# Kernel optimization log

Measured on AMD Instinct MI355X. Metric: run time of the kernel, lower is better.

Reference implementation:

```python
import jax, jax.numpy as jnp
import numpy as np

# KWConv2d config: in=256, out=256, k=3, s=1, p=1, groups=1, bias=False
# warehouse: 32 spatial cells of shape [64, 64, 3, 3]; num_fourier_basis=0; temp_value=0
B, CIN, H, W_ = 32, 256, 56, 56
OUT = 256
NUM_CELLS, CO, CI, KH, KW = 32, 64, 64, 3, 3
HIDDEN = 16                 # max(int(256 * 0.0625), 16)
GO, GI, GS = OUT // CO, CIN // CI, 1
M = GO * GI * GS            # num_local_mixture = 16
P = NUM_CELLS + 1           # kw_planes_per_mixture = 33
KWP = P * M                 # kw_planes = 528


def setup_inputs() -> dict:
    key = jax.random.key(0)
    ks = jax.random.split(key, 4)
    s = 0.02
    return {
        "x": jax.random.normal(ks[0], (B, CIN, H, W_), jnp.float32),
        "cells": jax.random.normal(ks[1], (NUM_CELLS, CO, CI, KH, KW), jnp.float32) * s,
        "fc1_w": jax.random.normal(ks[2], (HIDDEN, CIN), jnp.float32) * s,
        "fc1_b": jnp.zeros((HIDDEN,), jnp.float32),
        "ln_g": jnp.ones((HIDDEN,), jnp.float32),
        "ln_b": jnp.zeros((HIDDEN,), jnp.float32),
        "sp_w": jax.random.normal(ks[3], (KWP, HIDDEN), jnp.float32) * s,
        "sp_b": jnp.zeros((KWP,), jnp.float32),
    }


def _attention(x, fc1_w, fc1_b, ln_g, ln_b, sp_w, sp_b):
    # AdaptiveAvgPool1d(1) over flattened spatial dims == global mean
    pooled = x.mean(axis=(2, 3))                      # [B, CIN]
    h = pooled @ fc1_w.T + fc1_b                      # [B, HIDDEN]
    mu = h.mean(-1, keepdims=True)
    var = ((h - mu) ** 2).mean(-1, keepdims=True)
    h = (h - mu) * jax.lax.rsqrt(var + 1e-5) * ln_g + ln_b
    h = jax.nn.relu(h)
    a = h @ sp_w.T + sp_b                             # spatial_head -> [B, KWP]
    a = a.reshape(-1, P)                              # [B*M, P]
    a = a / (jnp.abs(a).sum(axis=1, keepdims=True) + 0.001)  # L1 normalize per mixture
    # temp_value = 0 -> attention unchanged; drop last (zero) column
    return a[:, :-1]                                  # [B*M, NUM_CELLS]


def reference(x, cells, fc1_w, fc1_b, ln_g, ln_b, sp_w, sp_b):
    att = _attention(x, fc1_w, fc1_b, ln_g, ln_b, sp_w, sp_b)  # [B*M, NUM_CELLS]
    w = cells.reshape(NUM_CELLS, -1)                  # [NUM_CELLS, CO*CI*KH*KW]
    agg = att @ w                                     # [B*M, CO*CI*KH*KW]
    agg = agg.reshape(B, GS, GO, GI, CO, CI, KH, KW)
    agg = agg.transpose(0, 2, 4, 3, 5, 1, 6, 7)       # torch permute (0,2,4,3,5,1,6,7)
    agg = agg.reshape(B * OUT, CIN, KH, KW)           # per-sample kernels (groups=1)
    # grouped-conv trick: fold batch into channels, groups = B
    xr = x.reshape(1, B * CIN, H, W_)
    out = jax.lax.conv_general_dilated(
        xr, agg, window_strides=(1, 1), padding=((1, 1), (1, 1)),
        dimension_numbers=("NCHW", "OIHW", "NCHW"), feature_group_count=B)
    return out.reshape(B, OUT, H, W_)
```

## Files before the change

kernel.cpp:

```cpp
#include <hip/hip_runtime.h>
#include <stdint.h>

typedef unsigned short ush;
typedef __bf16   bf16x8 __attribute__((ext_vector_type(8)));
typedef float    f32x4  __attribute__((ext_vector_type(4)));
typedef uint32_t u32x4  __attribute__((ext_vector_type(4)));

union U16B { u32x4 u; bf16x8 b; };
union P8   { ush us[8]; u32x4 v; };

__device__ __forceinline__ ush f2bf(float f) {
    union { float f; uint32_t u; } v; v.f = f;
    uint32_t r = v.u + 0x7FFFu + ((v.u >> 16) & 1u);
    return (ush)(r >> 16);
}

__device__ __forceinline__ void gl_lds16(const ush* g, ush* l) {
    __builtin_amdgcn_global_load_lds(
        (const __attribute__((address_space(1))) uint32_t*)g,
        (__attribute__((address_space(3))) uint32_t*)l, 16, 0, 0);
}

#define HWPX  3136
#define POOL_OFF   58720256UL
#define ATT_OFF    58753024UL
#define WAGG_OFF   58818560UL

__global__ void k_halo(u32x4* __restrict__ xT16, u32x4* __restrict__ pooled16) {
    int i = blockIdx.x * 256 + threadIdx.x;
    int rl = i >> 3, s = i & 7;
    u32x4 z = (u32x4)(0u);
    size_t byte = (size_t)rl * 4096 + (s < 4 ? s * 16 : 3648 + (s - 4) * 16);
    xT16[byte >> 4] = z;
    if (blockIdx.x < 8) pooled16[blockIdx.x * 256 + threadIdx.x] = z;
}

__global__ void k_transpose(const float* __restrict__ x, ush* __restrict__ xT,
                            float* __restrict__ pooled) {
    __shared__ float tile[64][65];
    int blk = blockIdx.x;
    int b   = blk / 196;
    int rem = blk % 196;
    int icg = rem / 49;
    int pxg = rem % 49;
    int t = threadIdx.x;

    {
        int icl  = t >> 2, part = t & 3;
        const float* src = x + (size_t)(b * 256 + icg * 64 + icl) * HWPX + pxg * 64 + part * 16;
        #pragma unroll
        for (int k = 0; k < 4; ++k) {
            f32x4 v = *(const f32x4*)(src + k * 4);
            tile[icl][part * 16 + k * 4 + 0] = v[0];
            tile[icl][part * 16 + k * 4 + 1] = v[1];
            tile[icl][part * 16 + k * 4 + 2] = v[2];
            tile[icl][part * 16 + k * 4 + 3] = v[3];
        }
    }
    __syncthreads();

    if (t < 64) {
        float s = 0.f;
        #pragma unroll 8
        for (int p = 0; p < 64; ++p) s += tile[t][p];
        atomicAdd(pooled + b * 256 + icg * 64 + t, s);
    }

    {
        int pxl = t >> 2, icq = t & 3;
        int px  = pxg * 64 + pxl;
        int row = px / 56;
        int col = px - row * 56;
        int p   = col + 1;
        int xorp = (p >> 1) & 3;
        int icg32   = icg * 2 + (icq >> 1);
        int subbase = (icq & 1) * 2;
        P8 lo, hi;
        #pragma unroll
        for (int m = 0; m < 8; ++m) {
            lo.us[m] = f2bf(tile[icq * 16 + m][pxl]);
            hi.us[m] = f2bf(tile[icq * 16 + 8 + m][pxl]);
        }
        size_t base = (((size_t)(b * 8 + icg32) * 56 + row) * 64 + p) * 32;
        *(u32x4*)(xT + base + (size_t)((subbase ^ xorp) * 8))       = lo.v;
        *(u32x4*)(xT + base + (size_t)(((subbase + 1) ^ xorp) * 8)) = hi.v;
    }
}

__global__ void k_attn(const float* __restrict__ pooled,
                       const float* __restrict__ fc1_w, const float* __restrict__ fc1_b,
                       const float* __restrict__ ln_g,  const float* __restrict__ ln_b,
                       const float* __restrict__ sp_w,  const float* __restrict__ sp_b,
                       float* __restrict__ att) {
    __shared__ float hs[32][16];
    int t = threadIdx.x;
    {
        int b = t >> 4, j = t & 15;
        float acc = 0.f;
        for (int c = 0; c < 256; ++c) acc += pooled[b * 256 + c] * fc1_w[j * 256 + c];
        hs[b][j] = fc1_b[j] + acc * (1.0f / 3136.0f);
    }
    __syncthreads();
    if (t < 32) {
        float mu = 0.f;
        #pragma unroll
        for (int j = 0; j < 16; ++j) mu += hs[t][j];
        mu *= (1.0f / 16.0f);
        float var = 0.f;
        #pragma unroll
        for (int j = 0; j < 16; ++j) { float d = hs[t][j] - mu; var += d * d; }
        var *= (1.0f / 16.0f);
        float inv = rsqrtf(var + 1e-5f);
        #pragma unroll
        for (int j = 0; j < 16; ++j) {
            float v = (hs[t][j] - mu) * inv * ln_g[j] + ln_b[j];
            hs[t][j] = fmaxf(v, 0.f);
        }
    }
    __syncthreads();
    {
        int b = t >> 4, m = t & 15;
        float a[33];
        #pragma unroll 1
        for (int i = 0; i < 33; ++i) {
            int p = m * 33 + i;
            float acc = sp_b[p];
            #pragma unroll
            for (int j = 0; j < 16; ++j) acc += hs[b][j] * sp_w[p * 16 + j];
            a[i] = acc;
        }
        float s = 0.f;
        #pragma unroll
        for (int i = 0; i < 33; ++i) s += fabsf(a[i]);
        float inv = 1.0f / (s + 0.001f);
        #pragma unroll
        for (int c = 0; c < 32; ++c) att[(b * 16 + m) * 32 + c] = a[c] * inv;
    }
}

__global__ void k_agg(const float* __restrict__ cells, const float* __restrict__ att,
                      ush* __restrict__ wagg) {
    __shared__ float at[512];
    int blk = blockIdx.x;
    int b = blk >> 6, co = blk & 63;
    int t = threadIdx.x;
    for (int i = t; i < 512; i += 256) at[i] = att[b * 512 + i];
    __syncthreads();
    int ci = t & 63, gi = t >> 6;
    float acc[4][9];
    #pragma unroll
    for (int g = 0; g < 4; ++g)
        #pragma unroll
        for (int k = 0; k < 9; ++k) acc[g][k] = 0.f;
    for (int c = 0; c < 32; ++c) {
        float a0 = at[(0 + gi) * 32 + c];
        float a1 = at[(4 + gi) * 32 + c];
        float a2 = at[(8 + gi) * 32 + c];
        float a3 = at[(12 + gi) * 32 + c];
        const float* cp = cells + (size_t)c * 36864 + co * 576 + ci * 9;
        #pragma unroll
        for (int k = 0; k < 9; ++k) {
            float cv = cp[k];
            acc[0][k] += a0 * cv; acc[1][k] += a1 * cv;
            acc[2][k] += a2 * cv; acc[3][k] += a3 * cv;
        }
    }
    #pragma unroll
    for (int g = 0; g < 4; ++g)
        #pragma unroll
        for (int k = 0; k < 9; ++k)
            wagg[((size_t)(b * 9 + k) * 256 + g * 64 + co) * 256 + gi * 64 + ci] = f2bf(acc[g][k]);
}

__global__ __launch_bounds__(256, 2) void k_conv(const ush* __restrict__ xT,
                                                 const ush* __restrict__ wagg,
                                                 float* __restrict__ out) {
    __shared__ __align__(16) ush xs[20480];
    __shared__ __align__(16) ush wsh[18432];

    int tid = threadIdx.x;
    int wg  = blockIdx.x;
    int xcd = wg & 7;
    int kk  = wg >> 3;
    int gq  = kk / 7;
    int sp  = kk - gq * 7;
    int g   = gq * 8 + xcd;
    int b   = g >> 2, octile = g & 3;
    int row0 = sp * 8, oc0 = octile * 64;

    int lane = tid & 63, w = tid >> 6;
    int l15 = lane & 15, s4 = lane >> 4;

    {
        u32x4 z = (u32x4)(0u);
        #pragma unroll
        for (int i = 0; i < 10; ++i) ((u32x4*)xs)[tid + i * 256] = z;
    }

    int prow[7], pq[7];
    #pragma unroll
    for (int j = 0; j < 7; ++j) {
        int px = w * 112 + j * 16 + l15;
        prow[j] = px / 56;
        pq[j]   = px - prow[j] * 56;
    }

    unsigned vmask = 0;
    #pragma unroll
    for (int k = 0; k < 10; ++k) {
        int grow = row0 - 1 + k;
        if (grow >= 0 && grow < 56) vmask |= 1u << k;
    }

    const ush* wgl = wagg + (size_t)b * 9 * 65536 + (size_t)(oc0 + (tid >> 2)) * 256 + (tid & 3) * 8;
    ush* wdst = wsh + ((tid & 3) * 64 + (tid >> 2)) * 8;
    const ush* wrd = wsh + (s4 * 64 + l15) * 8;
    const ush* xb = xT + (size_t)b * 8 * 56 * 2048 + (size_t)tid * 8;

    f32x4 acc[4][7];
    #pragma unroll
    for (int mi = 0; mi < 4; ++mi)
        #pragma unroll
        for (int j = 0; j < 7; ++j) acc[mi][j] = (f32x4)(0.f);

    __syncthreads();

    if ((wg >> 8) & 1) __builtin_amdgcn_s_sleep(32);

    for (int cc = 0; cc < 8; ++cc) {
        U16B wst[9];
        const ush* wcg = wgl + (size_t)cc * 32;
        #pragma unroll
        for (int k = 0; k < 9; ++k) wst[k].u = *(const u32x4*)(wcg + (size_t)k * 65536);
        #pragma unroll
        for (int k = 0; k < 10; ++k)
            if (vmask & (1u << k))
                gl_lds16(xb + (size_t)(cc * 56 + row0 - 1 + k) * 2048, xs + k * 2048 + w * 512);
        #pragma unroll
        for (int k = 0; k < 9; ++k) *(u32x4*)(wdst + k * 2048) = wst[k].u;
        __syncthreads();

        #pragma unroll
        for (int tap = 0; tap < 9; ++tap) {
            const int dy = tap / 3, dx = tap % 3;
            U16B wf[4];
            #pragma unroll
            for (int mi = 0; mi < 4; ++mi)
                wf[mi].u = *(const u32x4*)(wrd + tap * 2048 + mi * 128);
            U16B bx[7];
            #pragma unroll
            for (int j = 0; j < 7; ++j) {
                int q    = pq[j] + dx;
                int slot = s4 ^ ((q >> 1) & 3);
                bx[j].u = *(const u32x4*)(xs + ((prow[j] + dy) * 64 + q) * 32 + slot * 8);
            }
            __builtin_amdgcn_s_setprio(1);
            #pragma unroll
            for (int j = 0; j < 7; ++j) {
                acc[0][j] = __builtin_amdgcn_mfma_f32_16x16x32_bf16(bx[j].b, wf[0].b, acc[0][j], 0, 0, 0);
                acc[1][j] = __builtin_amdgcn_mfma_f32_16x16x32_bf16(bx[j].b, wf[1].b, acc[1][j], 0, 0, 0);
                acc[2][j] = __builtin_amdgcn_mfma_f32_16x16x32_bf16(bx[j].b, wf[2].b, acc[2][j], 0, 0, 0);
                acc[3][j] = __builtin_amdgcn_mfma_f32_16x16x32_bf16(bx[j].b, wf[3].b, acc[3][j], 0, 0, 0);
            }
            __builtin_amdgcn_s_setprio(0);
        }
        __syncthreads();
    }

    int pxbase = row0 * 56 + w * 112 + s4 * 4;
    #pragma unroll
    for (int mi = 0; mi < 4; ++mi) {
        int oc = oc0 + mi * 16 + l15;
        float* o = out + (size_t)(b * 256 + oc) * HWPX + pxbase;
        #pragma unroll
        for (int j = 0; j < 7; ++j)
            *(f32x4*)(o + j * 16) = acc[mi][j];
    }
}

extern "C" void kernel_launch(void* const* d_in, const int* in_sizes, int n_in,
                              void* d_out, int out_size, void* d_ws, size_t ws_size,
                              hipStream_t stream) {
    const float* x     = (const float*)d_in[0];
    const float* cells = (const float*)d_in[1];
    const float* fc1_w = (const float*)d_in[2];
    const float* fc1_b = (const float*)d_in[3];
    const float* ln_g  = (const float*)d_in[4];
    const float* ln_b  = (const float*)d_in[5];
    const float* sp_w  = (const float*)d_in[6];
    const float* sp_b  = (const float*)d_in[7];
    float* out = (float*)d_out;

    char* ws = (char*)d_ws;
    ush*   xT     = (ush*)ws;
    float* pooled = (float*)(ws + POOL_OFF);
    float* att    = (float*)(ws + ATT_OFF);
    ush*   wagg   = (ush*)(ws + WAGG_OFF);

    k_halo<<<448, 256, 0, stream>>>((u32x4*)ws, (u32x4*)pooled);
    k_transpose<<<6272, 256, 0, stream>>>(x, xT, pooled);
    k_attn<<<1, 512, 0, stream>>>(pooled, fc1_w, fc1_b, ln_g, ln_b, sp_w, sp_b, att);
    k_agg<<<2048, 256, 0, stream>>>(cells, att, wagg);
    k_conv<<<896, 256, 0, stream>>>(xT, wagg, out);
}
```

Baseline: 237.4 us.

## Double-buffer conv input tiles and widen workgroups to 128 output channels

The conv kernel now runs 512-thread workgroups that cover 128 output channels, so each x tile loaded into LDS is reused by twice as many channels and the grid shrinks to 448 blocks. The x halo tiles are double-buffered, and the weights for the next input-channel chunk are prefetched into registers while the current chunk computes. This hides global-load latency behind the MFMA work. In exchange it uses more LDS per block, allows only one block per CU, adds XOR swizzling to the weight layout, and replaces one barrier with manual waitcnt/barrier sequencing.

```diff
diff --git a/kernel.cpp b/kernel.cpp
--- a/kernel.cpp
+++ b/kernel.cpp
@@ -172,11 +172,11 @@
             wagg[((size_t)(b * 9 + k) * 256 + g * 64 + co) * 256 + gi * 64 + ci] = f2bf(acc[g][k]);
 }
 
-__global__ __launch_bounds__(256, 2) void k_conv(const ush* __restrict__ xT,
+__global__ __launch_bounds__(512, 1) void k_conv(const ush* __restrict__ xT,
                                                  const ush* __restrict__ wagg,
                                                  float* __restrict__ out) {
-    __shared__ __align__(16) ush xs[20480];
-    __shared__ __align__(16) ush wsh[18432];
+    __shared__ __align__(16) ush xs[2][20480];
+    __shared__ __align__(16) ush wsh[36864];
 
     int tid = threadIdx.x;
     int wg  = blockIdx.x;
@@ -185,22 +185,23 @@
     int gq  = kk / 7;
     int sp  = kk - gq * 7;
     int g   = gq * 8 + xcd;
-    int b   = g >> 2, octile = g & 3;
-    int row0 = sp * 8, oc0 = octile * 64;
+    int b   = g >> 1, octile = g & 1;
+    int row0 = sp * 8, oc0 = octile * 128;
 
     int lane = tid & 63, w = tid >> 6;
+    int ocH = w & 1, pxq = w >> 1;
     int l15 = lane & 15, s4 = lane >> 4;
 
     {
         u32x4 z = (u32x4)(0u);
         #pragma unroll
-        for (int i = 0; i < 10; ++i) ((u32x4*)xs)[tid + i * 256] = z;
+        for (int i = 0; i < 10; ++i) ((u32x4*)xs)[tid + i * 512] = z;
     }
 
     int prow[7], pq[7];
     #pragma unroll
     for (int j = 0; j < 7; ++j) {
-        int px = w * 112 + j * 16 + l15;
+        int px = pxq * 112 + j * 16 + l15;
         prow[j] = px / 56;
         pq[j]   = px - prow[j] * 56;
     }
@@ -213,9 +214,10 @@
     }
 
     const ush* wgl = wagg + (size_t)b * 9 * 65536 + (size_t)(oc0 + (tid >> 2)) * 256 + (tid & 3) * 8;
-    ush* wdst = wsh + ((tid & 3) * 64 + (tid >> 2)) * 8;
-    const ush* wrd = wsh + (s4 * 64 + l15) * 8;
-    const ush* xb = xT + (size_t)b * 8 * 56 * 2048 + (size_t)tid * 8;
+    ush* wdst = wsh + (tid & 3) * 1024 + (((tid >> 2) ^ ((tid & 3) << 2)) << 3);
+    const ush* wrd = wsh + s4 * 1024 + (((ocH << 6) + (l15 ^ (s4 << 2))) << 3);
+    int xl = tid & 255, xh = tid >> 8;
+    const ush* xb = xT + (size_t)b * 8 * 56 * 2048 + (size_t)xl * 8;
 
     f32x4 acc[4][7];
     #pragma unroll
@@ -225,34 +227,47 @@
 
     __syncthreads();
 
-    if ((wg >> 8) & 1) __builtin_amdgcn_s_sleep(32);
+    U16B wpre[9];
+    #pragma unroll
+    for (int k = 0; k < 9; ++k) wpre[k].u = *(const u32x4*)(wgl + (size_t)k * 65536);
+    #pragma unroll
+    for (int r = 0; r < 5; ++r) {
+        int row = r * 2 + xh;
+        if ((vmask >> row) & 1)
+            gl_lds16(xb + (size_t)(row0 - 1 + row) * 2048, &xs[0][0] + row * 2048 + xl * 8);
+    }
+    #pragma unroll
+    for (int k = 0; k < 9; ++k) *(u32x4*)(wdst + k * 4096) = wpre[k].u;
+    __syncthreads();
 
     for (int cc = 0; cc < 8; ++cc) {
-        U16B wst[9];
-        const ush* wcg = wgl + (size_t)cc * 32;
-        #pragma unroll
-        for (int k = 0; k < 9; ++k) wst[k].u = *(const u32x4*)(wcg + (size_t)k * 65536);
-        #pragma unroll
-        for (int k = 0; k < 10; ++k)
-            if (vmask & (1u << k))
-                gl_lds16(xb + (size_t)(cc * 56 + row0 - 1 + k) * 2048, xs + k * 2048 + w * 512);
-        #pragma unroll
-        for (int k = 0; k < 9; ++k) *(u32x4*)(wdst + k * 2048) = wst[k].u;
-        __syncthreads();
-
+        if (cc < 7) {
+            const ush* wgc = wgl + (size_t)(cc + 1) * 32;
+            #pragma unroll
+            for (int k = 0; k < 9; ++k) wpre[k].u = *(const u32x4*)(wgc + (size_t)k * 65536);
+            ush* xdst = &xs[0][0] + ((cc & 1) ^ 1) * 20480;
+            #pragma unroll
+            for (int r = 0; r < 5; ++r) {
+                int row = r * 2 + xh;
+                if ((vmask >> row) & 1)
+                    gl_lds16(xb + (size_t)((cc + 1) * 56 + row0 - 1 + row) * 2048,
+                             xdst + row * 2048 + xl * 8);
+            }
+        }
+        const ush* xsb = &xs[0][0] + (cc & 1) * 20480;
         #pragma unroll
         for (int tap = 0; tap < 9; ++tap) {
             const int dy = tap / 3, dx = tap % 3;
             U16B wf[4];
             #pragma unroll
             for (int mi = 0; mi < 4; ++mi)
-                wf[mi].u = *(const u32x4*)(wrd + tap * 2048 + mi * 128);
+                wf[mi].u = *(const u32x4*)(wrd + tap * 4096 + mi * 128);
             U16B bx[7];
             #pragma unroll
             for (int j = 0; j < 7; ++j) {
                 int q    = pq[j] + dx;
                 int slot = s4 ^ ((q >> 1) & 3);
-                bx[j].u = *(const u32x4*)(xs + ((prow[j] + dy) * 64 + q) * 32 + slot * 8);
+                bx[j].u = *(const u32x4*)(xsb + ((prow[j] + dy) * 64 + q) * 32 + slot * 8);
             }
             __builtin_amdgcn_s_setprio(1);
             #pragma unroll
@@ -264,13 +279,21 @@
             }
             __builtin_amdgcn_s_setprio(0);
         }
-        __syncthreads();
-    }
-
-    int pxbase = row0 * 56 + w * 112 + s4 * 4;
+        asm volatile("s_waitcnt lgkmcnt(0)" ::: "memory");
+        __builtin_amdgcn_s_barrier();
+        if (cc < 7) {
+            #pragma unroll
+            for (int k = 0; k < 9; ++k) *(u32x4*)(wdst + k * 4096) = wpre[k].u;
+            asm volatile("s_waitcnt vmcnt(0)" ::: "memory");
+            asm volatile("s_waitcnt lgkmcnt(0)" ::: "memory");
+            __builtin_amdgcn_s_barrier();
+        }
+    }
+
+    int pxbase = row0 * 56 + pxq * 112 + s4 * 4;
     #pragma unroll
     for (int mi = 0; mi < 4; ++mi) {
-        int oc = oc0 + mi * 16 + l15;
+        int oc = oc0 + ocH * 64 + mi * 16 + l15;
         float* o = out + (size_t)(b * 256 + oc) * HWPX + pxbase;
         #pragma unroll
         for (int j = 0; j < 7; ++j)
@@ -301,5 +324,5 @@
     k_transpose<<<6272, 256, 0, stream>>>(x, xT, pooled);
     k_attn<<<1, 512, 0, stream>>>(pooled, fc1_w, fc1_b, ln_g, ln_b, sp_w, sp_b, att);
     k_agg<<<2048, 256, 0, stream>>>(cells, att, wagg);
-    k_conv<<<896, 256, 0, stream>>>(xT, wagg, out);
-}
+    k_conv<<<448, 512, 0, stream>>>(xT, wagg, out);
+}
```

After: 328.8 us. 1.39x slower.
